# Kernel optimization log

Hardware: AMD Instinct MI355X
Metric: run time of the kernel (lower is better)

Reference implementation:

```python
import jax, jax.numpy as jnp
import numpy as np

BN_EPS = 1e-5
W_EPS = 1e-8


def knn(query_xyz, key_xyz, k):
    # squared euclidean distances [B, Nq, Nk] via ||a||^2 + ||b||^2 - 2 a.b
    d = (jnp.sum(query_xyz ** 2, -1)[:, :, None]
         + jnp.sum(key_xyz ** 2, -1)[:, None, :]
         - 2.0 * jnp.einsum('bnd,bsd->bns', query_xyz, key_xyz))
    neg_d, idx = jax.lax.top_k(-d, k)  # k smallest distances
    return -neg_d, idx


def mlp_layer(x, w, b, g, beta):
    # Conv1d(kernel=1) == pointwise matmul; x: [B, N, Cin], w: [Cout, Cin]
    y = jnp.einsum('bnc,oc->bno', x, w) + b
    mean = jnp.mean(y, axis=(0, 1))          # BatchNorm1d training stats
    var = jnp.var(y, axis=(0, 1))            # biased variance (torch default)
    y = (y - mean) * jax.lax.rsqrt(var + BN_EPS) * g + beta
    return jax.nn.relu(y)


def setup_inputs() -> dict:
    key = jax.random.key(0)
    ks = jax.random.split(key, 12)
    B, S, N = 4, 4096, 16384
    Cs, Co = 256, 128
    Cin = Cs + Co
    C1, C2 = 256, 256
    return {
        'sampled_xyz': jax.random.normal(ks[0], (B, S, 3), jnp.float32),
        'sampled_features': jax.random.normal(ks[1], (B, S, Cs), jnp.float32),
        'original_xyz': jax.random.normal(ks[2], (B, N, 3), jnp.float32),
        'original_features': jax.random.normal(ks[3], (B, N, Co), jnp.float32),
        'w0': jax.random.normal(ks[4], (C1, Cin), jnp.float32) * (1.0 / np.sqrt(Cin)),
        'b0': jax.random.normal(ks[5], (C1,), jnp.float32) * 0.01,
        'g0': jnp.ones((C1,), jnp.float32),
        'bt0': jnp.zeros((C1,), jnp.float32),
        'w1': jax.random.normal(ks[6], (C2, C1), jnp.float32) * (1.0 / np.sqrt(C1)),
        'b1': jax.random.normal(ks[7], (C2,), jnp.float32) * 0.01,
        'g1': jnp.ones((C2,), jnp.float32),
        'bt1': jnp.zeros((C2,), jnp.float32),
        'k': 3,
    }


def reference(sampled_xyz, sampled_features, original_xyz, original_features,
              w0, b0, g0, bt0, w1, b1, g1, bt1, k):
    knn_dists, knn_idx = knn(original_xyz, sampled_xyz, k)      # [B, N, k]
    knn_w = 1.0 / (knn_dists + W_EPS)
    knn_w = knn_w / jnp.sum(knn_w, axis=-1, keepdims=True)
    # gather sampled features per neighbor: [B, N, k, Cs]
    knn_feats = jax.vmap(lambda f, i: f[i])(sampled_features, knn_idx)
    interp = jnp.sum(knn_feats * knn_w[:, :, :, None], axis=2)  # [B, N, Cs]
    x = jnp.concatenate([original_features, interp], axis=-1)    # [B, N, Co+Cs]
    x = mlp_layer(x, w0, b0, g0, bt0)
    x = mlp_layer(x, w1, b1, g1, bt1)
    return x
```

## Files before the change

kernel.cpp:

```cpp
#include <hip/hip_runtime.h>
#include <hip/hip_bf16.h>
#include <cstdint>
#include <cstddef>

#define Bn   4
#define Sn   4096
#define Nn   16384
#define CSn  256
#define COn  128
#define CINn 384
#define MTOT 65536

using short8 = short __attribute__((ext_vector_type(8)));
using f32x4  = float __attribute__((ext_vector_type(4)));
using f32x2  = float __attribute__((ext_vector_type(2)));

static __device__ __forceinline__ float bf2f(unsigned short u){
  unsigned int x = ((unsigned int)u) << 16;
  return __builtin_bit_cast(float, x);
}
static __device__ __forceinline__ unsigned short f2bf(float f){
  unsigned int x = __builtin_bit_cast(unsigned int, f);
  x += 0x7fffu + ((x >> 16) & 1u);
  return (unsigned short)(x >> 16);
}

static __device__ __forceinline__ void top3_insert(float d, int s,
    float& d0, float& d1, float& d2, int& i0, int& i1, int& i2){
  if (d < d2){
    if (d < d1){
      d2 = d1; i2 = i1;
      if (d < d0){ d1 = d0; i1 = i0; d0 = d; i0 = s; }
      else       { d1 = d;  i1 = s; }
    } else { d2 = d; i2 = s; }
  }
}

__global__ __launch_bounds__(256) void knn_kernel(
    const float* __restrict__ sxyz, const float* __restrict__ oxyz,
    float* __restrict__ PD, int* __restrict__ PI)
{
  __shared__ float4 cb[4][2][2][64];

  const int b    = blockIdx.x >> 9;
  const int qblk = (blockIdx.x >> 1) & 255;
  const int half = blockIdx.x & 1;
  const int lane = threadIdx.x & 63;
  const int wave = threadIdx.x >> 6;
  const int gq   = b*Nn + qblk*64 + lane;
  const float* op = oxyz + (size_t)gq*3;
  const float px = op[0], py = op[1], pz = op[2];
  const float qq = __fadd_rn(__fadd_rn(__fmul_rn(px,px), __fmul_rn(py,py)), __fmul_rn(pz,pz));
  const f32x2 px2 = {px,px}, py2 = {py,py}, pz2 = {pz,pz}, qq2 = {qq,qq};
  const f32x2 m2  = {-2.0f,-2.0f};

  const float* sx = sxyz + (size_t)b*Sn*3;
  const int slice = half*4 + wave;
  const int sbase = half*2048 + wave*512;

  float ax, ay, az, bx, by, bz;
  {
    int ja = sbase + lane, jb = ja + 256;
    ax=sx[ja*3+0]; ay=sx[ja*3+1]; az=sx[ja*3+2];
    bx=sx[jb*3+0]; by=sx[jb*3+1]; bz=sx[jb*3+2];
  }
  {
    float assv = __fadd_rn(__fadd_rn(__fmul_rn(ax,ax), __fmul_rn(ay,ay)), __fmul_rn(az,az));
    float bssv = __fadd_rn(__fadd_rn(__fmul_rn(bx,bx), __fmul_rn(by,by)), __fmul_rn(bz,bz));
    cb[wave][0][0][lane] = make_float4(ax, bx, ay, by);
    cb[wave][0][1][lane] = make_float4(az, bz, assv, bssv);
  }

  float dA0=3.4e38f,dA1=3.4e38f,dA2=3.4e38f; int iA0=0,iA1=0,iA2=0;
  float dB0=3.4e38f,dB1=3.4e38f,dB2=3.4e38f; int iB0=0,iB1=0,iB2=0;

  int cur = 0;
  for (int c = 0; c < 4; ++c){
    if (c < 3){
      int ja = sbase + (c+1)*64 + lane, jb = ja + 256;
      ax=sx[ja*3+0]; ay=sx[ja*3+1]; az=sx[ja*3+2];
      bx=sx[jb*3+0]; by=sx[jb*3+1]; bz=sx[jb*3+2];
    }
    const int base = sbase + c*64;
    #pragma unroll 8
    for (int i = 0; i < 64; ++i){
      float4 lo = cb[wave][cur][0][i];
      float4 hi = cb[wave][cur][1][i];
      f32x2 kx  = {lo.x, lo.y};
      f32x2 ky  = {lo.z, lo.w};
      f32x2 kz  = {hi.x, hi.y};
      f32x2 kss = {hi.z, hi.w};
      f32x2 dot, dd;
      asm("v_pk_mul_f32 %0, %2, %6\n\t"
          "v_pk_fma_f32 %0, %3, %7, %0\n\t"
          "v_pk_fma_f32 %0, %4, %8, %0\n\t"
          "v_pk_add_f32 %1, %9, %5\n\t"
          "v_pk_fma_f32 %1, %10, %0, %1"
          : "=&v"(dot), "=&v"(dd)
          : "v"(kx), "v"(ky), "v"(kz), "v"(kss),
            "v"(px2), "v"(py2), "v"(pz2), "v"(qq2), "v"(m2));
      const float ddA = dd.x, ddB = dd.y;
      {
        unsigned long long c0, c1, c2; int t;
        asm("v_cmp_lt_f32 %[c0], %[dd], %[d0]\n\t"
            "v_cmp_lt_f32 %[c1], %[dd], %[d1]\n\t"
            "v_cmp_lt_f32 %[c2], %[dd], %[d2]\n\t"
            "v_med3_f32 %[d2], %[dd], %[d1], %[d2]\n\t"
            "v_med3_f32 %[d1], %[dd], %[d0], %[d1]\n\t"
            "v_min_f32  %[d0], %[dd], %[d0]\n\t"
            "v_cndmask_b32 %[t], %[idx], %[i1], %[c1]\n\t"
            "v_cndmask_b32 %[i2], %[i2], %[t], %[c2]\n\t"
            "v_cndmask_b32 %[t], %[idx], %[i0], %[c0]\n\t"
            "v_cndmask_b32 %[i1], %[i1], %[t], %[c1]\n\t"
            "v_cndmask_b32 %[i0], %[i0], %[idx], %[c0]"
            : [d0]"+v"(dA0), [d1]"+v"(dA1), [d2]"+v"(dA2),
              [i0]"+v"(iA0), [i1]"+v"(iA1), [i2]"+v"(iA2),
              [t]"=&v"(t), [c0]"=&s"(c0), [c1]"=&s"(c1), [c2]"=&s"(c2)
            : [dd]"v"(ddA), [idx]"v"(base + i));
      }
      {
        unsigned long long c0, c1, c2; int t;
        asm("v_cmp_lt_f32 %[c0], %[dd], %[d0]\n\t"
            "v_cmp_lt_f32 %[c1], %[dd], %[d1]\n\t"
            "v_cmp_lt_f32 %[c2], %[dd], %[d2]\n\t"
            "v_med3_f32 %[d2], %[dd], %[d1], %[d2]\n\t"
            "v_med3_f32 %[d1], %[dd], %[d0], %[d1]\n\t"
            "v_min_f32  %[d0], %[dd], %[d0]\n\t"
            "v_cndmask_b32 %[t], %[idx], %[i1], %[c1]\n\t"
            "v_cndmask_b32 %[i2], %[i2], %[t], %[c2]\n\t"
            "v_cndmask_b32 %[t], %[idx], %[i0], %[c0]\n\t"
            "v_cndmask_b32 %[i1], %[i1], %[t], %[c1]\n\t"
            "v_cndmask_b32 %[i0], %[i0], %[idx], %[c0]"
            : [d0]"+v"(dB0), [d1]"+v"(dB1), [d2]"+v"(dB2),
              [i0]"+v"(iB0), [i1]"+v"(iB1), [i2]"+v"(iB2),
              [t]"=&v"(t), [c0]"=&s"(c0), [c1]"=&s"(c1), [c2]"=&s"(c2)
            : [dd]"v"(ddB), [idx]"v"(base + i + 256));
      }
    }
    if (c < 3){
      int nxt = cur ^ 1;
      float assv = __fadd_rn(__fadd_rn(__fmul_rn(ax,ax), __fmul_rn(ay,ay)), __fmul_rn(az,az));
      float bssv = __fadd_rn(__fadd_rn(__fmul_rn(bx,bx), __fmul_rn(by,by)), __fmul_rn(bz,bz));
      cb[wave][nxt][0][lane] = make_float4(ax, bx, ay, by);
      cb[wave][nxt][1][lane] = make_float4(az, bz, assv, bssv);
      cur = nxt;
    }
  }

  top3_insert(dB0, iB0, dA0,dA1,dA2, iA0,iA1,iA2);
  top3_insert(dB1, iB1, dA0,dA1,dA2, iA0,iA1,iA2);
  top3_insert(dB2, iB2, dA0,dA1,dA2, iA0,iA1,iA2);
  PD[(slice*3+0)*MTOT + gq] = dA0;
  PD[(slice*3+1)*MTOT + gq] = dA1;
  PD[(slice*3+2)*MTOT + gq] = dA2;
  PI[(slice*3+0)*MTOT + gq] = iA0;
  PI[(slice*3+1)*MTOT + gq] = iA1;
  PI[(slice*3+2)*MTOT + gq] = iA2;
}

__global__ __launch_bounds__(256) void knnmerge_kernel(
    const float* __restrict__ PD, const int* __restrict__ PI,
    float* __restrict__ kw, int* __restrict__ ki)
{
  const int gq = blockIdx.x*256 + threadIdx.x;
  float e0=3.4e38f, e1=3.4e38f, e2=3.4e38f;
  int   j0=0, j1=0, j2=0;
  #pragma unroll
  for (int s = 0; s < 8; ++s){
    #pragma unroll
    for (int j = 0; j < 3; ++j){
      float d = PD[(s*3+j)*MTOT + gq];
      int   i = PI[(s*3+j)*MTOT + gq];
      top3_insert(d, i, e0,e1,e2, j0,j1,j2);
    }
  }
  float wa = 1.0f/(e0+1e-8f), wb = 1.0f/(e1+1e-8f), wc = 1.0f/(e2+1e-8f);
  float sm = __fadd_rn(__fadd_rn(wa, wb), wc);
  size_t base = (size_t)gq*3;
  kw[base+0] = wa/sm; kw[base+1] = wb/sm; kw[base+2] = wc/sm;
  ki[base+0] = j0;    ki[base+1] = j1;    ki[base+2] = j2;
}

__global__ __launch_bounds__(256) void interp_kernel(
    const float* __restrict__ sfeat, const float* __restrict__ ofeat,
    const float* __restrict__ kw, const int* __restrict__ ki,
    unsigned short* __restrict__ X)
{
  const int c  = threadIdx.x;
  const int m0 = blockIdx.x * 16;
  for (int p = 0; p < 16; ++p){
    const int m = m0 + p;
    const int b = m >> 14;
    const float w0v = kw[(size_t)m*3+0], w1v = kw[(size_t)m*3+1], w2v = kw[(size_t)m*3+2];
    const int   i0  = ki[(size_t)m*3+0], i1  = ki[(size_t)m*3+1], i2  = ki[(size_t)m*3+2];
    const float* sb = sfeat + (size_t)b * Sn * CSn;
    float v = __fmaf_rn(w2v, sb[(size_t)i2*CSn + c],
              __fmaf_rn(w1v, sb[(size_t)i1*CSn + c],
              __fmul_rn(w0v, sb[(size_t)i0*CSn + c])));
    X[(size_t)m*CINn + COn + c] = f2bf(v);
    if (c < COn) X[(size_t)m*CINn + c] = f2bf(ofeat[(size_t)m*COn + c]);
  }
}

__global__ __launch_bounds__(256) void cvtw_kernel(
    const float* __restrict__ w0, const float* __restrict__ w1,
    unsigned short* __restrict__ w0b, unsigned short* __restrict__ w1b)
{
  int i = blockIdx.x*256 + threadIdx.x;
  if (i < 256*384) w0b[i] = f2bf(w0[i]);
  int j = i - 256*384;
  if (j >= 0 && j < 256*256) w1b[j] = f2bf(w1[j]);
}

template<int KDIM, bool BNRELU>
__global__ __launch_bounds__(256) void gemm_kernel(
    const unsigned short* __restrict__ A,
    const unsigned short* __restrict__ W,
    const float* __restrict__ bias,
    const float* __restrict__ s0sum,
    const float* __restrict__ s0sq,
    const float* __restrict__ bng,
    const float* __restrict__ bnbt,
    unsigned short* __restrict__ Y,
    float* __restrict__ osum,
    float* __restrict__ osq)
{
  __shared__ unsigned short As[128*64];
  __shared__ unsigned short Bs[256*64];
  __shared__ float lsc[256], lsh[256];
  const int tid  = threadIdx.x;
  const int lane = tid & 63;
  const int wave = tid >> 6;
  const size_t mbase = (size_t)blockIdx.x * 128;
  if constexpr (BNRELU){
    float mean = s0sum[tid] * (1.0f/65536.0f);
    float var  = s0sq[tid] * (1.0f/65536.0f) - mean*mean;
    float s = bng[tid] / sqrtf(var + 1e-5f);
    lsc[tid] = s;
    lsh[tid] = __fmaf_rn(-mean, s, bnbt[tid]);
  }
  f32x4 acc[8][4];
  #pragma unroll
  for (int m2 = 0; m2 < 8; ++m2)
    #pragma unroll
    for (int n2 = 0; n2 < 4; ++n2) acc[m2][n2] = f32x4{0.f,0.f,0.f,0.f};
  __syncthreads();

  for (int k0 = 0; k0 < KDIM; k0 += 64){
    if (k0) __syncthreads();
    #pragma unroll
    for (int i = 0; i < 4; ++i){
      int cid = tid + 256*i;
      int row = cid >> 3, c8 = cid & 7;
      short8 v = *reinterpret_cast<const short8*>(A + (mbase+row)*KDIM + k0 + c8*8);
      if constexpr (BNRELU){
        #pragma unroll
        for (int j = 0; j < 8; ++j){
          int kc = k0 + c8*8 + j;
          float f = bf2f((unsigned short)v[j]);
          f = fmaxf(__fmaf_rn(f, lsc[kc], lsh[kc]), 0.0f);
          v[j] = (short)f2bf(f);
        }
      }
      *reinterpret_cast<short8*>(reinterpret_cast<char*>(As) + row*128 + ((c8 ^ (row&7)) << 4)) = v;
    }
    #pragma unroll
    for (int i = 0; i < 8; ++i){
      int cid = tid + 256*i;
      int row = cid >> 3, c8 = cid & 7;
      short8 v = *reinterpret_cast<const short8*>(W + (size_t)row*KDIM + k0 + c8*8);
      *reinterpret_cast<short8*>(reinterpret_cast<char*>(Bs) + row*128 + ((c8 ^ (row&7)) << 4)) = v;
    }
    __syncthreads();
    #pragma unroll
    for (int kk = 0; kk < 2; ++kk){
      short8 af[8], bv[4];
      #pragma unroll
      for (int m2 = 0; m2 < 8; ++m2){
        int row = m2*16 + (lane & 15);
        int c8  = kk*4 + (lane >> 4);
        af[m2] = *reinterpret_cast<const short8*>(reinterpret_cast<char*>(As) + row*128 + ((c8 ^ (row&7)) << 4));
      }
      #pragma unroll
      for (int n2 = 0; n2 < 4; ++n2){
        int row = wave*64 + n2*16 + (lane & 15);
        int c8  = kk*4 + (lane >> 4);
        bv[n2] = *reinterpret_cast<const short8*>(reinterpret_cast<char*>(Bs) + row*128 + ((c8 ^ (row&7)) << 4));
      }
      #pragma unroll
      for (int m2 = 0; m2 < 8; ++m2)
        #pragma unroll
        for (int n2 = 0; n2 < 4; ++n2)
          acc[m2][n2] = __builtin_amdgcn_mfma_f32_16x16x32_bf16(af[m2], bv[n2], acc[m2][n2], 0, 0, 0);
    }
  }

  const int colg0 = wave*64;
  float spart[4] = {0,0,0,0}, qpart[4] = {0,0,0,0};
  #pragma unroll
  for (int m2 = 0; m2 < 8; ++m2){
    #pragma unroll
    for (int n2 = 0; n2 < 4; ++n2){
      const int gc  = colg0 + n2*16 + (lane & 15);
      const float bvv = bias[gc];
      #pragma unroll
      for (int j = 0; j < 4; ++j){
        float yv = acc[m2][n2][j] + bvv;
        size_t gr = mbase + m2*16 + (lane>>4)*4 + j;
        Y[gr*256 + gc] = f2bf(yv);
        spart[n2] += yv;
        qpart[n2] = __fmaf_rn(yv, yv, qpart[n2]);
      }
    }
  }
  #pragma unroll
  for (int n2 = 0; n2 < 4; ++n2){
    float s = spart[n2], q = qpart[n2];
    s += __shfl_xor(s, 16); q += __shfl_xor(q, 16);
    s += __shfl_xor(s, 32); q += __shfl_xor(q, 32);
    if (lane < 16){
      int gc = colg0 + n2*16 + lane;
      atomicAdd(&osum[gc], s);
      atomicAdd(&osq[gc], q);
    }
  }
}

__global__ __launch_bounds__(256) void apply_kernel(
    const unsigned short* __restrict__ y,
    const float* __restrict__ s1sum, const float* __restrict__ s1sq,
    const float* __restrict__ g, const float* __restrict__ bt,
    float* __restrict__ out)
{
  __shared__ float ssc[256], ssh[256];
  {
    int c = threadIdx.x;
    float mean = s1sum[c] * (1.0f/65536.0f);
    float var  = s1sq[c] * (1.0f/65536.0f) - mean*mean;
    float s = g[c] / sqrtf(var + 1e-5f);
    ssc[c] = s;
    ssh[c] = __fmaf_rn(-mean, s, bt[c]);
  }
  __syncthreads();
  const int t = blockIdx.x*256 + threadIdx.x;
  const size_t base = (size_t)t * 8;
  const int c0 = (int)(base & 255);
  short8 v = *reinterpret_cast<const short8*>(y + base);
  float r[8];
  #pragma unroll
  for (int j = 0; j < 8; ++j){
    float f = bf2f((unsigned short)v[j]);
    f = __fmaf_rn(f, ssc[c0+j], ssh[c0+j]);
    r[j] = fmaxf(f, 0.0f);
  }
  float4 o0, o1;
  o0.x=r[0]; o0.y=r[1]; o0.z=r[2]; o0.w=r[3];
  o1.x=r[4]; o1.y=r[5]; o1.z=r[6]; o1.w=r[7];
  *reinterpret_cast<float4*>(out + base)     = o0;
  *reinterpret_cast<float4*>(out + base + 4) = o1;
}

constexpr size_t WS_STATS = 0;
constexpr size_t WS_W0B   = 8192;
constexpr size_t WS_W1B   = WS_W0B + 196608;
constexpr size_t WS_KW    = WS_W1B + 131072;
constexpr size_t WS_KI    = WS_KW + 786432;
constexpr size_t WS_X     = 4194304;
constexpr size_t WS_Y0    = WS_X + (size_t)MTOT*CINn*2;
constexpr size_t WS_PD    = WS_X;
constexpr size_t WS_PI    = WS_X + (size_t)8*3*MTOT*4;

extern "C" void kernel_launch(void* const* d_in, const int* in_sizes, int n_in,
                              void* d_out, int out_size, void* d_ws, size_t ws_size,
                              hipStream_t stream)
{
  const float* sxyz  = (const float*)d_in[0];
  const float* sfeat = (const float*)d_in[1];
  const float* oxyz  = (const float*)d_in[2];
  const float* ofeat = (const float*)d_in[3];
  const float* w0    = (const float*)d_in[4];
  const float* b0    = (const float*)d_in[5];
  const float* g0    = (const float*)d_in[6];
  const float* bt0   = (const float*)d_in[7];
  const float* w1    = (const float*)d_in[8];
  const float* b1    = (const float*)d_in[9];
  const float* g1    = (const float*)d_in[10];
  const float* bt1   = (const float*)d_in[11];

  char* ws = (char*)d_ws;
  float* stats  = (float*)(ws + WS_STATS);
  unsigned short* w0b = (unsigned short*)(ws + WS_W0B);
  unsigned short* w1b = (unsigned short*)(ws + WS_W1B);
  float* kw = (float*)(ws + WS_KW);
  int*   ki = (int*)(ws + WS_KI);
  float* PD = (float*)(ws + WS_PD);
  int*   PI = (int*)(ws + WS_PI);
  unsigned short* X  = (unsigned short*)(ws + WS_X);
  unsigned short* Y0 = (unsigned short*)(ws + WS_Y0);
  unsigned short* Y1 = (unsigned short*)(ws + WS_X);

  hipMemsetAsync(stats, 0, 4*256*sizeof(float), stream);
  cvtw_kernel<<<640, 256, 0, stream>>>(w0, w1, w0b, w1b);
  knn_kernel<<<2048, 256, 0, stream>>>(sxyz, oxyz, PD, PI);
  knnmerge_kernel<<<MTOT/256, 256, 0, stream>>>(PD, PI, kw, ki);
  interp_kernel<<<MTOT/16, 256, 0, stream>>>(sfeat, ofeat, kw, ki, X);
  gemm_kernel<CINn, false><<<MTOT/128, 256, 0, stream>>>(
      X, w0b, b0, nullptr, nullptr, nullptr, nullptr, Y0, stats, stats + 256);
  gemm_kernel<256, true><<<MTOT/128, 256, 0, stream>>>(
      Y0, w1b, b1, stats, stats + 256, g0, bt0, Y1, stats + 512, stats + 768);
  apply_kernel<<<(MTOT*256)/(256*8), 256, 0, stream>>>(
      Y1, stats + 512, stats + 768, g1, bt1, (float*)d_out);
}
```

Measured before the change: 262.5 us.

## Fuse kNN feature interpolation and concat into first GEMM's A-tile load

Removes the separate interp kernel and the bf16 X intermediate buffer. The first GEMM now builds its A tile on the fly: it reads original features directly and forms interpolated sampled features from three gathered rows weighted by kNN weights staged in shared memory. This avoids writing and re-reading a 65536x384 bf16 matrix and saves one launch. In exchange the GEMM's load phase carries gather latency and extra FP32 reads inside its main loop.

After: 240.4 us. 8.4% less time.

```diff
diff --git a/kernel.cpp b/kernel.cpp
--- a/kernel.cpp
+++ b/kernel.cpp
@@ -181,27 +181,6 @@
   ki[base+0] = j0;    ki[base+1] = j1;    ki[base+2] = j2;
 }
 
-__global__ __launch_bounds__(256) void interp_kernel(
-    const float* __restrict__ sfeat, const float* __restrict__ ofeat,
-    const float* __restrict__ kw, const int* __restrict__ ki,
-    unsigned short* __restrict__ X)
-{
-  const int c  = threadIdx.x;
-  const int m0 = blockIdx.x * 16;
-  for (int p = 0; p < 16; ++p){
-    const int m = m0 + p;
-    const int b = m >> 14;
-    const float w0v = kw[(size_t)m*3+0], w1v = kw[(size_t)m*3+1], w2v = kw[(size_t)m*3+2];
-    const int   i0  = ki[(size_t)m*3+0], i1  = ki[(size_t)m*3+1], i2  = ki[(size_t)m*3+2];
-    const float* sb = sfeat + (size_t)b * Sn * CSn;
-    float v = __fmaf_rn(w2v, sb[(size_t)i2*CSn + c],
-              __fmaf_rn(w1v, sb[(size_t)i1*CSn + c],
-              __fmul_rn(w0v, sb[(size_t)i0*CSn + c])));
-    X[(size_t)m*CINn + COn + c] = f2bf(v);
-    if (c < COn) X[(size_t)m*CINn + c] = f2bf(ofeat[(size_t)m*COn + c]);
-  }
-}
-
 __global__ __launch_bounds__(256) void cvtw_kernel(
     const float* __restrict__ w0, const float* __restrict__ w1,
     unsigned short* __restrict__ w0b, unsigned short* __restrict__ w1b)
@@ -212,7 +191,7 @@
   if (j >= 0 && j < 256*256) w1b[j] = f2bf(w1[j]);
 }
 
-template<int KDIM, bool BNRELU>
+template<int KDIM, bool BNRELU, bool AFUSE>
 __global__ __launch_bounds__(256) void gemm_kernel(
     const unsigned short* __restrict__ A,
     const unsigned short* __restrict__ W,
@@ -221,6 +200,10 @@
     const float* __restrict__ s0sq,
     const float* __restrict__ bng,
     const float* __restrict__ bnbt,
+    const float* __restrict__ kwg,
+    const int*   __restrict__ kig,
+    const float* __restrict__ sfeat,
+    const float* __restrict__ ofeat,
     unsigned short* __restrict__ Y,
     float* __restrict__ osum,
     float* __restrict__ osq)
@@ -228,6 +211,8 @@
   __shared__ unsigned short As[128*64];
   __shared__ unsigned short Bs[256*64];
   __shared__ float lsc[256], lsh[256];
+  __shared__ float lkw[128][3];
+  __shared__ int   lki[128][3];
   const int tid  = threadIdx.x;
   const int lane = tid & 63;
   const int wave = tid >> 6;
@@ -239,6 +224,14 @@
     lsc[tid] = s;
     lsh[tid] = __fmaf_rn(-mean, s, bnbt[tid]);
   }
+  if constexpr (AFUSE){
+    float* lkwf = &lkw[0][0];
+    int*   lkif = &lki[0][0];
+    for (int t = tid; t < 384; t += 256){
+      lkwf[t] = kwg[mbase*3 + t];
+      lkif[t] = kig[mbase*3 + t];
+    }
+  }
   f32x4 acc[8][4];
   #pragma unroll
   for (int m2 = 0; m2 < 8; ++m2)
@@ -252,14 +245,47 @@
     for (int i = 0; i < 4; ++i){
       int cid = tid + 256*i;
       int row = cid >> 3, c8 = cid & 7;
-      short8 v = *reinterpret_cast<const short8*>(A + (mbase+row)*KDIM + k0 + c8*8);
-      if constexpr (BNRELU){
+      short8 v;
+      if constexpr (AFUSE){
+        const int m = (int)mbase + row;
+        const int k = k0 + c8*8;
+        float vals[8];
+        if (k < COn){
+          const float4* p = reinterpret_cast<const float4*>(ofeat + (size_t)m*COn + k);
+          float4 u0 = p[0], u1 = p[1];
+          vals[0]=u0.x; vals[1]=u0.y; vals[2]=u0.z; vals[3]=u0.w;
+          vals[4]=u1.x; vals[5]=u1.y; vals[6]=u1.z; vals[7]=u1.w;
+        } else {
+          const int cc = k - COn;
+          const int bb = m >> 14;
+          const float* sb = sfeat + (size_t)bb*Sn*CSn;
+          const float w0v = lkw[row][0], w1v = lkw[row][1], w2v = lkw[row][2];
+          const int   i0  = lki[row][0], i1  = lki[row][1], i2  = lki[row][2];
+          const float4* p0 = reinterpret_cast<const float4*>(sb + (size_t)i0*CSn + cc);
+          const float4* p1 = reinterpret_cast<const float4*>(sb + (size_t)i1*CSn + cc);
+          const float4* p2 = reinterpret_cast<const float4*>(sb + (size_t)i2*CSn + cc);
+          float4 a0 = p0[0], a1 = p0[1];
+          float4 b0v = p1[0], b1v = p1[1];
+          float4 c0v = p2[0], c1v = p2[1];
+          float s0[8] = {a0.x,a0.y,a0.z,a0.w,a1.x,a1.y,a1.z,a1.w};
+          float s1[8] = {b0v.x,b0v.y,b0v.z,b0v.w,b1v.x,b1v.y,b1v.z,b1v.w};
+          float s2[8] = {c0v.x,c0v.y,c0v.z,c0v.w,c1v.x,c1v.y,c1v.z,c1v.w};
+          #pragma unroll
+          for (int j = 0; j < 8; ++j)
+            vals[j] = __fmaf_rn(w2v, s2[j], __fmaf_rn(w1v, s1[j], __fmul_rn(w0v, s0[j])));
+        }
         #pragma unroll
-        for (int j = 0; j < 8; ++j){
-          int kc = k0 + c8*8 + j;
-          float f = bf2f((unsigned short)v[j]);
-          f = fmaxf(__fmaf_rn(f, lsc[kc], lsh[kc]), 0.0f);
-          v[j] = (short)f2bf(f);
+        for (int j = 0; j < 8; ++j) v[j] = (short)f2bf(vals[j]);
+      } else {
+        v = *reinterpret_cast<const short8*>(A + (mbase+row)*KDIM + k0 + c8*8);
+        if constexpr (BNRELU){
+          #pragma unroll
+          for (int j = 0; j < 8; ++j){
+            int kc = k0 + c8*8 + j;
+            float f = bf2f((unsigned short)v[j]);
+            f = fmaxf(__fmaf_rn(f, lsc[kc], lsh[kc]), 0.0f);
+            v[j] = (short)f2bf(f);
+          }
         }
       }
       *reinterpret_cast<short8*>(reinterpret_cast<char*>(As) + row*128 + ((c8 ^ (row&7)) << 4)) = v;
@@ -365,10 +391,10 @@
 constexpr size_t WS_W1B   = WS_W0B + 196608;
 constexpr size_t WS_KW    = WS_W1B + 131072;
 constexpr size_t WS_KI    = WS_KW + 786432;
-constexpr size_t WS_X     = 4194304;
-constexpr size_t WS_Y0    = WS_X + (size_t)MTOT*CINn*2;
-constexpr size_t WS_PD    = WS_X;
-constexpr size_t WS_PI    = WS_X + (size_t)8*3*MTOT*4;
+constexpr size_t WS_BIG   = 4194304;
+constexpr size_t WS_Y0    = WS_BIG + (size_t)MTOT*CINn*2;
+constexpr size_t WS_PD    = WS_BIG;
+constexpr size_t WS_PI    = WS_BIG + (size_t)8*3*MTOT*4;
 
 extern "C" void kernel_launch(void* const* d_in, const int* in_sizes, int n_in,
                               void* d_out, int out_size, void* d_ws, size_t ws_size,
@@ -395,19 +421,19 @@
   int*   ki = (int*)(ws + WS_KI);
   float* PD = (float*)(ws + WS_PD);
   int*   PI = (int*)(ws + WS_PI);
-  unsigned short* X  = (unsigned short*)(ws + WS_X);
   unsigned short* Y0 = (unsigned short*)(ws + WS_Y0);
-  unsigned short* Y1 = (unsigned short*)(ws + WS_X);
+  unsigned short* Y1 = (unsigned short*)(ws + WS_BIG);
 
   hipMemsetAsync(stats, 0, 4*256*sizeof(float), stream);
   cvtw_kernel<<<640, 256, 0, stream>>>(w0, w1, w0b, w1b);
   knn_kernel<<<2048, 256, 0, stream>>>(sxyz, oxyz, PD, PI);
   knnmerge_kernel<<<MTOT/256, 256, 0, stream>>>(PD, PI, kw, ki);
-  interp_kernel<<<MTOT/16, 256, 0, stream>>>(sfeat, ofeat, kw, ki, X);
-  gemm_kernel<CINn, false><<<MTOT/128, 256, 0, stream>>>(
-      X, w0b, b0, nullptr, nullptr, nullptr, nullptr, Y0, stats, stats + 256);
-  gemm_kernel<256, true><<<MTOT/128, 256, 0, stream>>>(
-      Y0, w1b, b1, stats, stats + 256, g0, bt0, Y1, stats + 512, stats + 768);
+  gemm_kernel<CINn, false, true><<<MTOT/128, 256, 0, stream>>>(
+      nullptr, w0b, b0, nullptr, nullptr, nullptr, nullptr,
+      kw, ki, sfeat, ofeat, Y0, stats, stats + 256);
+  gemm_kernel<256, true, false><<<MTOT/128, 256, 0, stream>>>(
+      Y0, w1b, b1, stats, stats + 256, g0, bt0,
+      nullptr, nullptr, nullptr, nullptr, Y1, stats + 512, stats + 768);
   apply_kernel<<<(MTOT*256)/(256*8), 256, 0, stream>>>(
       Y1, stats + 512, stats + 768, g1, bt1, (float*)d_out);
 }
```
